# Optimization experiments

Hardware: AMD Instinct MI355X
Metric: run time of the kernel (lower is better)

The kernel has to match this reference:

```python
import jax, jax.numpy as jnp
import numpy as np

N, K, D, H, DK, DV, E = 20000, 20, 128, 4, 32, 32, 128
HID = 4 * D


def _ln(x, g, b, eps=1e-5):
    m = x.mean(-1, keepdims=True)
    v = ((x - m) ** 2).mean(-1, keepdims=True)
    return (x - m) / jnp.sqrt(v + eps) * g + b


def setup_inputs() -> dict:
    key = jax.random.key(0)
    ks = jax.random.split(key, 24)
    inp = {
        "node_h_src": jax.random.normal(ks[0], (N, K, D), jnp.float32),
        "t": jax.random.uniform(ks[1], (N, K), jnp.float32),
        "t_now": jnp.ones((1,), jnp.float32),
        "edge_feat": jax.random.normal(ks[2], (N, K, E), jnp.float32),
        # time-encoding params (as in __init__)
        "basis_freq": jnp.asarray(1.0 / 10 ** np.linspace(0, 9, D), jnp.float32),
        "phase": jnp.zeros((D,), jnp.float32),
        # edge_fc
        "edge_fc_w": jax.random.normal(ks[3], (E, D), jnp.float32) * 0.05,
        "edge_fc_b": jnp.zeros((D,), jnp.float32),
        # QKV projections (stored as [in, out])
        "w_qs": jax.random.normal(ks[4], (D, H * DK), jnp.float32) * np.sqrt(2.0 / (D + DK)),
        "w_ks": jax.random.normal(ks[5], (D, H * DK), jnp.float32) * np.sqrt(2.0 / (D + DK)),
        "w_vs": jax.random.normal(ks[6], (D, H * DV), jnp.float32) * np.sqrt(2.0 / (D + DV)),
        "w_qs_src": jax.random.normal(ks[7], (D, H * DK), jnp.float32) * np.sqrt(2.0 / (D + DK)),
        # attn output fc
        "attn_fc_w": jax.random.normal(ks[8], (H * DV, D), jnp.float32) * 0.05,
        "attn_fc_b": jnp.zeros((D,), jnp.float32),
        "attn_ln_g": jnp.ones((D,), jnp.float32),
        "attn_ln_b": jnp.zeros((D,), jnp.float32),
        # positionwise FFN (Conv1d kernel 1 == linear)
        "ffn_w1": jax.random.normal(ks[9], (D, HID), jnp.float32) * 0.05,
        "ffn_b1": jnp.zeros((HID,), jnp.float32),
        "ffn_w2": jax.random.normal(ks[10], (HID, D), jnp.float32) * 0.05,
        "ffn_b2": jnp.zeros((D,), jnp.float32),
        "ffn_ln_g": jnp.ones((D,), jnp.float32),
        "ffn_ln_b": jnp.zeros((D,), jnp.float32),
        # fuse + output norm
        "fea2node_w": jax.random.normal(ks[11], (2 * D, D), jnp.float32) * 0.05,
        "fea2node_b": jnp.zeros((D,), jnp.float32),
        "out_ln_g": jnp.ones((D,), jnp.float32),
        "out_ln_b": jnp.zeros((D,), jnp.float32),
    }
    return inp


def reference(node_h_src, t, t_now, edge_feat, basis_freq, phase,
              edge_fc_w, edge_fc_b, w_qs, w_ks, w_vs, w_qs_src,
              attn_fc_w, attn_fc_b, attn_ln_g, attn_ln_b,
              ffn_w1, ffn_b1, ffn_w2, ffn_b2, ffn_ln_g, ffn_ln_b,
              fea2node_w, fea2node_b, out_ln_g, out_ln_b):
    gelu = lambda x: jax.nn.gelu(x, approximate=False)
    # message: temporal encoding + edge feature fusion
    t_enc = jnp.cos((t_now - t)[..., None] * basis_freq + phase)          # [N,K,D]
    z = node_h_src + gelu(edge_feat @ edge_fc_w + edge_fc_b) + t_enc      # [N,K,D]
    q = z @ w_qs                                                          # [N,K,H*DK]
    k = z @ w_ks
    v = z @ w_vs
    # reduce: self message replaces last slot. NOTE: original code uses
    # self_q for q, k AND v (w_ks_src/w_vs_src unused) -- reproduced faithfully.
    self_q = (z[:, -1, :] @ w_qs_src)[:, None, :]                         # [N,1,H*DK]
    q = jnp.concatenate([q[:, :-1, :], self_q], axis=1)
    k = jnp.concatenate([k[:, :-1, :], self_q], axis=1)
    v = jnp.concatenate([v[:, :-1, :], self_q], axis=1)
    qh = q.reshape(N, K, H, DK)
    kh = k.reshape(N, K, H, DK)
    vh = v.reshape(N, K, H, DV)
    attn = jnp.einsum("nqhd,nkhd->nhqk", qh, kh) / jnp.sqrt(jnp.float32(DK))
    attn = jax.nn.softmax(attn, axis=-1)
    out = jnp.einsum("nhqk,nkhd->nqhd", attn, vh).reshape(N, K, H * DV)
    out = out @ attn_fc_w + attn_fc_b
    x = _ln(out + z, attn_ln_g, attn_ln_b)                                # [N,K,D]
    # positionwise FFN with residual + LN
    ffn = jax.nn.relu(x @ ffn_w1 + ffn_b1) @ ffn_w2 + ffn_b2
    x = _ln(ffn + x, ffn_ln_g, ffn_ln_b)
    # fuse self slot with mean of neighbor slots
    neighborhood = x[:, :-1, :].mean(axis=1)                              # [N,D]
    fused = jnp.concatenate([x[:, -1, :], neighborhood], axis=-1)         # [N,2D]
    node_h = _ln(gelu(fused @ fea2node_w + fea2node_b) + node_h_src[:, -1, :],
                 out_ln_g, out_ln_b)
    return node_h
```

## Files before the change

### kernel.cpp

```cpp
#include <hip/hip_runtime.h>
#include <hip/hip_bf16.h>

#define N_NODES 20000
#define KK 20
#define DD 128
#define HH 4
#define DKK 32
#define EE 128
#define HIDD 512
#define RTOT (N_NODES * KK)

using bf16 = __hip_bfloat16;

typedef short s16x8 __attribute__((ext_vector_type(8)));
typedef float f32x4 __attribute__((ext_vector_type(4)));

__device__ __forceinline__ float geluf(float x) {
    return 0.5f * x * (1.0f + erff(x * 0.70710678118654752f));
}

__device__ __forceinline__ float wave_sum(float v) {
#pragma unroll
    for (int o = 32; o > 0; o >>= 1) v += __shfl_down(v, o);
    return __shfl(v, 0);
}

__global__ __launch_bounds__(256)
void k0_conv(const float* __restrict__ w1, const float* __restrict__ w2,
             bf16* __restrict__ w1t, bf16* __restrict__ w2t)
{
    const int id = blockIdx.x * 256 + threadIdx.x;
    if (id < HIDD * DD) {
        const int n = id / DD, k = id % DD;
        w1t[id] = __float2bfloat16(w1[k * HIDD + n]);
    } else {
        const int j = id - HIDD * DD;
        const int n = j / HIDD, k = j % HIDD;
        w2t[j] = __float2bfloat16(w2[k * DD + n]);
    }
}

__global__ __launch_bounds__(256)
void k0b_conv(const float* __restrict__ wq, const float* __restrict__ wk,
              const float* __restrict__ wv, const float* __restrict__ wqs,
              const float* __restrict__ afw, const float* __restrict__ ew,
              bf16* __restrict__ aw)
{
    const int id = blockIdx.x * 256 + threadIdx.x;
    const int m = id >> 14;
    const int r = id & 16383;
    const int n = r >> 7, k = r & 127;
    const float* src = (m == 0) ? wq : (m == 1) ? wk : (m == 2) ? wv
                     : (m == 3) ? wqs : (m == 4) ? afw : ew;
    aw[id] = __float2bfloat16(src[k * DD + n]);
}

__global__ __launch_bounds__(256)
void k1_msg(const float* __restrict__ nhs, const float* __restrict__ t,
            const float* __restrict__ t_now, const float* __restrict__ ef,
            const float* __restrict__ freq, const float* __restrict__ phase,
            const bf16* __restrict__ ewt, const float* __restrict__ eb,
            bf16* __restrict__ z)
{
    __shared__ bf16  efs[32][136];
    __shared__ float gs[32][132];
    __shared__ float ts[32];

    const int tid  = threadIdx.x;
    const int wv   = tid >> 6;
    const int lane = tid & 63;
    const int col  = lane & 15;
    const int quad = lane >> 4;
    const size_t base = (size_t)blockIdx.x * 32 * DD;

    {
        const float4* src = (const float4*)(ef + base);
#pragma unroll
        for (int it = 0; it < 4; it++) {
            const int i = tid + it * 256;
            const int r = i >> 5, c = (i & 31) * 4;
            const float4 v = src[i];
            bf16 tmp[4] = { __float2bfloat16(v.x), __float2bfloat16(v.y),
                            __float2bfloat16(v.z), __float2bfloat16(v.w) };
            *(uint2*)&efs[r][c] = *(const uint2*)tmp;
        }
    }
    if (tid < 32) ts[tid] = t[blockIdx.x * 32 + tid];
    __syncthreads();

    {
        f32x4 acc[2][2];
#pragma unroll
        for (int mt = 0; mt < 2; mt++)
#pragma unroll
            for (int nt = 0; nt < 2; nt++) acc[mt][nt] = (f32x4){0.f, 0.f, 0.f, 0.f};

#pragma unroll
        for (int kk = 0; kk < 4; kk++) {
            const int k0 = kk * 32 + quad * 8;
            const s16x8 a0 = *(const s16x8*)&efs[col][k0];
            const s16x8 a1 = *(const s16x8*)&efs[16 + col][k0];
#pragma unroll
            for (int nt = 0; nt < 2; nt++) {
                const int n = wv * 32 + nt * 16 + col;
                const s16x8 b = *(const s16x8*)&ewt[n * DD + k0];
                acc[0][nt] = __builtin_amdgcn_mfma_f32_16x16x32_bf16(a0, b, acc[0][nt], 0, 0, 0);
                acc[1][nt] = __builtin_amdgcn_mfma_f32_16x16x32_bf16(a1, b, acc[1][nt], 0, 0, 0);
            }
        }

#pragma unroll
        for (int mt = 0; mt < 2; mt++)
#pragma unroll
            for (int nt = 0; nt < 2; nt++) {
                const int n = wv * 32 + nt * 16 + col;
                const float bias = eb[n];
#pragma unroll
                for (int r = 0; r < 4; r++) {
                    const int row = mt * 16 + quad * 4 + r;
                    gs[row][n] = geluf(acc[mt][nt][r] + bias);
                }
            }
    }
    __syncthreads();

    {
        const float tn = t_now[0];
        const float4* nsrc = (const float4*)(nhs + base);
#pragma unroll
        for (int it = 0; it < 4; it++) {
            const int i = tid + it * 256;
            const int r = i >> 5, c = (i & 31) * 4;
            const float4 h  = nsrc[i];
            const float4 fq = *(const float4*)&freq[c];
            const float4 ph = *(const float4*)&phase[c];
            const float dt  = tn - ts[r];
            const float o0 = h.x + gs[r][c + 0] + __cosf(dt * fq.x + ph.x);
            const float o1 = h.y + gs[r][c + 1] + __cosf(dt * fq.y + ph.y);
            const float o2 = h.z + gs[r][c + 2] + __cosf(dt * fq.z + ph.z);
            const float o3 = h.w + gs[r][c + 3] + __cosf(dt * fq.w + ph.w);
            bf16 o[4] = { __float2bfloat16(o0), __float2bfloat16(o1),
                          __float2bfloat16(o2), __float2bfloat16(o3) };
            *(uint2*)&z[base + r * DD + c] = *(const uint2*)o;
        }
    }
}

__global__ __launch_bounds__(256)
void k2_attn(bf16* __restrict__ zx, const bf16* __restrict__ aw,
             const float* __restrict__ afb,
             const float* __restrict__ lng, const float* __restrict__ lnb)
{
    __shared__ __align__(16) char smem[46784];
    bf16  (*zs)[136]     = (bf16  (*)[136])(smem);
    float (*qf)[132]     = (float (*)[132])(smem + 8704);
    float (*kf)[132]     = (float (*)[132])(smem + 19264);
    float (*vf)[132]     = (float (*)[132])(smem + 29824);
    float (*sc)[KK][KK]  = (float (*)[KK][KK])(smem + 40384);
    bf16  (*obf)[136]    = (bf16  (*)[136])(smem + 8704);
    float (*us)[132]     = (float (*)[132])(smem + 19264);

    const int t    = threadIdx.x;
    const int wv4  = t >> 6;
    const int lane = t & 63;
    const int col  = lane & 15;
    const int quad = lane >> 4;
    const int node = blockIdx.x;
    bf16* zrow = zx + node * KK * DD;

    const uint4 z4 = make_uint4(0u, 0u, 0u, 0u);

    {
        const uint4* src = (const uint4*)zrow;
        for (int i = t; i < 320; i += 256) {
            const int r = i >> 4, c = (i & 15) * 8;
            *(uint4*)&zs[r][c] = src[i];
        }
        for (int i = t; i < 204; i += 256) {
            const int r = 20 + i / 17, c = (i % 17) * 8;
            *(uint4*)&zs[r][c] = z4;
        }
    }
    __syncthreads();

    {
        const bf16* Wm = aw + wv4 * (DD * DD);
        f32x4 acc[2][8];
#pragma unroll
        for (int mt = 0; mt < 2; mt++)
#pragma unroll
            for (int nt = 0; nt < 8; nt++) acc[mt][nt] = (f32x4){0.f, 0.f, 0.f, 0.f};

#pragma unroll
        for (int kk = 0; kk < 4; kk++) {
            const int k0 = kk * 32 + quad * 8;
            const s16x8 a0 = *(const s16x8*)&zs[col][k0];
            const s16x8 a1 = *(const s16x8*)&zs[16 + col][k0];
#pragma unroll
            for (int nt = 0; nt < 8; nt++) {
                const s16x8 b = *(const s16x8*)&Wm[(nt * 16 + col) * DD + k0];
                acc[0][nt] = __builtin_amdgcn_mfma_f32_16x16x32_bf16(a0, b, acc[0][nt], 0, 0, 0);
                acc[1][nt] = __builtin_amdgcn_mfma_f32_16x16x32_bf16(a1, b, acc[1][nt], 0, 0, 0);
            }
        }

        if (wv4 < 3) {
            float (*dst)[132] = (wv4 == 0) ? qf : (wv4 == 1) ? kf : vf;
#pragma unroll
            for (int mt = 0; mt < 2; mt++)
#pragma unroll
                for (int nt = 0; nt < 8; nt++)
#pragma unroll
                    for (int r = 0; r < 4; r++) {
                        const int row = mt * 16 + quad * 4 + r;
                        if (row >= 19) continue;
                        dst[row][nt * 16 + col] = acc[mt][nt][r];
                    }
        } else if (quad == 0) {
#pragma unroll
            for (int nt = 0; nt < 8; nt++) {
                const int n = nt * 16 + col;
                const float s = acc[1][nt][3];
                qf[19][n] = s; kf[19][n] = s; vf[19][n] = s;
            }
        }
    }
    __syncthreads();

    const float scale = 0.17677669529663687f;
    for (int idx = t; idx < HH * KK * KK; idx += 256) {
        const int h = idx / (KK * KK);
        const int rem = idx % (KK * KK);
        const int i = rem / KK, j = rem % KK;
        float s = 0.f;
#pragma unroll
        for (int d = 0; d < DKK; d++)
            s += qf[i][h * DKK + d] * kf[j][h * DKK + d];
        sc[h][i][j] = s * scale;
    }
    __syncthreads();

    if (t < HH * KK) {
        const int h = t / KK, i = t % KK;
        float m = -1e30f;
#pragma unroll
        for (int j = 0; j < KK; j++) m = fmaxf(m, sc[h][i][j]);
        float s = 0.f;
#pragma unroll
        for (int j = 0; j < KK; j++) { const float e = __expf(sc[h][i][j] - m); sc[h][i][j] = e; s += e; }
        const float inv = 1.0f / s;
#pragma unroll
        for (int j = 0; j < KK; j++) sc[h][i][j] *= inv;
    }
    __syncthreads();

    for (int idx = t; idx < KK * DD; idx += 256) {
        const int i = idx / DD, c = idx % DD, h = c / DKK;
        float o = 0.f;
#pragma unroll
        for (int j = 0; j < KK; j++) o += sc[h][i][j] * vf[j][c];
        obf[i][c] = __float2bfloat16(o);
    }
    for (int i = t; i < 204; i += 256) {
        const int r = 20 + i / 17, c = (i % 17) * 8;
        *(uint4*)&obf[r][c] = z4;
    }
    __syncthreads();

    {
        const bf16* AF = aw + 4 * (DD * DD);
        f32x4 facc[2][2];
#pragma unroll
        for (int mt = 0; mt < 2; mt++)
#pragma unroll
            for (int nt = 0; nt < 2; nt++) facc[mt][nt] = (f32x4){0.f, 0.f, 0.f, 0.f};

#pragma unroll
        for (int kk = 0; kk < 4; kk++) {
            const int k0 = kk * 32 + quad * 8;
            const s16x8 a0 = *(const s16x8*)&obf[col][k0];
            const s16x8 a1 = *(const s16x8*)&obf[16 + col][k0];
#pragma unroll
            for (int nt = 0; nt < 2; nt++) {
                const int n = (wv4 * 2 + nt) * 16 + col;
                const s16x8 b = *(const s16x8*)&AF[n * DD + k0];
                facc[0][nt] = __builtin_amdgcn_mfma_f32_16x16x32_bf16(a0, b, facc[0][nt], 0, 0, 0);
                facc[1][nt] = __builtin_amdgcn_mfma_f32_16x16x32_bf16(a1, b, facc[1][nt], 0, 0, 0);
            }
        }

#pragma unroll
        for (int mt = 0; mt < 2; mt++)
#pragma unroll
            for (int nt = 0; nt < 2; nt++) {
                const int n = (wv4 * 2 + nt) * 16 + col;
                const float bias = afb[n];
#pragma unroll
                for (int r = 0; r < 4; r++) {
                    const int i = mt * 16 + quad * 4 + r;
                    if (i >= 20) continue;
                    us[i][n] = facc[mt][nt][r] + bias + __bfloat162float(zs[i][n]);
                }
            }
    }
    __syncthreads();

    for (int i = wv4; i < KK; i += 4) {
        const float a0 = us[i][lane], a1 = us[i][lane + 64];
        const float s  = wave_sum(a0 + a1);
        const float sq = wave_sum(a0 * a0 + a1 * a1);
        const float mean = s * (1.0f / DD);
        const float var  = sq * (1.0f / DD) - mean * mean;
        const float inv  = rsqrtf(var + 1e-5f);
        zrow[i * DD + lane]      = __float2bfloat16((a0 - mean) * inv * lng[lane] + lnb[lane]);
        zrow[i * DD + lane + 64] = __float2bfloat16((a1 - mean) * inv * lng[lane + 64] + lnb[lane + 64]);
    }
}

#define XPAD (DD + 8)
#define HPAD (HIDD + 8)

__global__ __launch_bounds__(256)
void k3_ffn(bf16* __restrict__ zx,
            const bf16* __restrict__ w1t, const float* __restrict__ b1,
            const bf16* __restrict__ w2t, const float* __restrict__ b2,
            const float* __restrict__ lng, const float* __restrict__ lnb)
{
    __shared__ bf16 xs[32][XPAD];
    __shared__ bf16 h1[32][HPAD];

    const int t    = threadIdx.x;
    const int wv   = t >> 6;
    const int lane = t & 63;
    const int col  = lane & 15;
    const int quad = lane >> 4;
    const int base = blockIdx.x * 32 * DD;

    {
        const uint4* src = (const uint4*)(zx + base);
#pragma unroll
        for (int it = 0; it < 2; it++) {
            const int i = t + it * 256;
            const int r = i >> 4, c = (i & 15) * 8;
            *(uint4*)&xs[r][c] = src[i];
        }
    }
    __syncthreads();

    {
        f32x4 acc[2][8];
#pragma unroll
        for (int mt = 0; mt < 2; mt++)
#pragma unroll
            for (int nt = 0; nt < 8; nt++) acc[mt][nt] = (f32x4){0.f, 0.f, 0.f, 0.f};

#pragma unroll
        for (int kk = 0; kk < 4; kk++) {
            const int k0 = kk * 32 + quad * 8;
            const s16x8 a0 = *(const s16x8*)&xs[col][k0];
            const s16x8 a1 = *(const s16x8*)&xs[16 + col][k0];
#pragma unroll
            for (int nt = 0; nt < 8; nt++) {
                const int n = wv * 128 + nt * 16 + col;
                const s16x8 b = *(const s16x8*)&w1t[n * DD + k0];
                acc[0][nt] = __builtin_amdgcn_mfma_f32_16x16x32_bf16(a0, b, acc[0][nt], 0, 0, 0);
                acc[1][nt] = __builtin_amdgcn_mfma_f32_16x16x32_bf16(a1, b, acc[1][nt], 0, 0, 0);
            }
        }
#pragma unroll
        for (int nt = 0; nt < 8; nt++) {
            const int n = wv * 128 + nt * 16 + col;
            const float bias = b1[n];
#pragma unroll
            for (int r = 0; r < 4; r++) {
                const int row = quad * 4 + r;
                h1[row][n]      = __float2bfloat16(fmaxf(acc[0][nt][r] + bias, 0.f));
                h1[16 + row][n] = __float2bfloat16(fmaxf(acc[1][nt][r] + bias, 0.f));
            }
        }
    }
    __syncthreads();

    {
        f32x4 acc[2][2];
#pragma unroll
        for (int mt = 0; mt < 2; mt++)
#pragma unroll
            for (int nt = 0; nt < 2; nt++) acc[mt][nt] = (f32x4){0.f, 0.f, 0.f, 0.f};

#pragma unroll 4
        for (int kk = 0; kk < 16; kk++) {
            const int k0 = kk * 32 + quad * 8;
            const s16x8 a0 = *(const s16x8*)&h1[col][k0];
            const s16x8 a1 = *(const s16x8*)&h1[16 + col][k0];
#pragma unroll
            for (int nt = 0; nt < 2; nt++) {
                const int n = wv * 32 + nt * 16 + col;
                const s16x8 b = *(const s16x8*)&w2t[n * HIDD + k0];
                acc[0][nt] = __builtin_amdgcn_mfma_f32_16x16x32_bf16(a0, b, acc[0][nt], 0, 0, 0);
                acc[1][nt] = __builtin_amdgcn_mfma_f32_16x16x32_bf16(a1, b, acc[1][nt], 0, 0, 0);
            }
        }
        __syncthreads();

        float* u = (float*)&h1[0][0];
#pragma unroll
        for (int mt = 0; mt < 2; mt++)
#pragma unroll
            for (int nt = 0; nt < 2; nt++) {
                const int n = wv * 32 + nt * 16 + col;
                const float bias = b2[n];
#pragma unroll
                for (int r = 0; r < 4; r++) {
                    const int row = mt * 16 + quad * 4 + r;
                    u[row * DD + n] = acc[mt][nt][r] + bias + __bfloat162float(xs[row][n]);
                }
            }
    }
    __syncthreads();

    {
        const float* u = (const float*)&h1[0][0];
        for (int r = wv; r < 32; r += 4) {
            const float a0 = u[r * DD + lane], a1 = u[r * DD + lane + 64];
            const float s  = wave_sum(a0 + a1);
            const float sq = wave_sum(a0 * a0 + a1 * a1);
            const float mean = s * (1.0f / DD);
            const float var  = sq * (1.0f / DD) - mean * mean;
            const float inv  = rsqrtf(var + 1e-5f);
            zx[base + r * DD + lane]      = __float2bfloat16((a0 - mean) * inv * lng[lane] + lnb[lane]);
            zx[base + r * DD + lane + 64] = __float2bfloat16((a1 - mean) * inv * lng[lane + 64] + lnb[lane + 64]);
        }
    }
}

__global__ __launch_bounds__(128)
void k4_fuse(const bf16* __restrict__ zx, const float* __restrict__ nhs,
             const float* __restrict__ fw, const float* __restrict__ fb,
             const float* __restrict__ lng, const float* __restrict__ lnb,
             float* __restrict__ out)
{
    __shared__ float f[2 * DD];
    __shared__ float red[4];
    const int d = threadIdx.x;
    const int node = blockIdx.x;
    const bf16* xr = zx + node * KK * DD;

    float nb = 0.f;
#pragma unroll
    for (int i = 0; i < KK - 1; i++) nb += __bfloat162float(xr[i * DD + d]);
    f[d] = __bfloat162float(xr[(KK - 1) * DD + d]);
    f[DD + d] = nb * (1.0f / (KK - 1));
    __syncthreads();

    float a = fb[d];
#pragma unroll 4
    for (int c = 0; c < 2 * DD; c++) a += f[c] * fw[c * DD + d];
    const float y = geluf(a) + nhs[(node * KK + KK - 1) * DD + d];

    float s = y, sq = y * y;
#pragma unroll
    for (int o = 32; o > 0; o >>= 1) {
        s += __shfl_down(s, o);
        sq += __shfl_down(sq, o);
    }
    const int wid = d >> 6, lane = d & 63;
    if (lane == 0) { red[wid] = s; red[2 + wid] = sq; }
    __syncthreads();
    const float ts = red[0] + red[1], tsq = red[2] + red[3];
    const float mean = ts * (1.0f / DD);
    const float var = tsq * (1.0f / DD) - mean * mean;
    const float inv = rsqrtf(var + 1e-5f);
    out[node * DD + d] = (y - mean) * inv * lng[d] + lnb[d];
}

extern "C" void kernel_launch(void* const* d_in, const int* in_sizes, int n_in,
                              void* d_out, int out_size, void* d_ws, size_t ws_size,
                              hipStream_t stream)
{
    const float* nhs   = (const float*)d_in[0];
    const float* t     = (const float*)d_in[1];
    const float* tnow  = (const float*)d_in[2];
    const float* ef    = (const float*)d_in[3];
    const float* freq  = (const float*)d_in[4];
    const float* phase = (const float*)d_in[5];
    const float* ew    = (const float*)d_in[6];
    const float* eb    = (const float*)d_in[7];
    const float* wq    = (const float*)d_in[8];
    const float* wk    = (const float*)d_in[9];
    const float* wv    = (const float*)d_in[10];
    const float* wqs   = (const float*)d_in[11];
    const float* afw   = (const float*)d_in[12];
    const float* afb   = (const float*)d_in[13];
    const float* alng  = (const float*)d_in[14];
    const float* alnb  = (const float*)d_in[15];
    const float* w1    = (const float*)d_in[16];
    const float* b1    = (const float*)d_in[17];
    const float* w2    = (const float*)d_in[18];
    const float* b2    = (const float*)d_in[19];
    const float* flng  = (const float*)d_in[20];
    const float* flnb  = (const float*)d_in[21];
    const float* fw    = (const float*)d_in[22];
    const float* fb    = (const float*)d_in[23];
    const float* olng  = (const float*)d_in[24];
    const float* olnb  = (const float*)d_in[25];
    float* out = (float*)d_out;

    bf16* zx  = (bf16*)d_ws;
    bf16* w1t = (bf16*)((char*)d_ws + (size_t)RTOT * DD * 2);
    bf16* w2t = w1t + HIDD * DD;
    bf16* aw  = w2t + DD * HIDD;
    bf16* ewt = aw + 5 * DD * DD;

    k0_conv<<<dim3(2 * HIDD * DD / 256), dim3(256), 0, stream>>>(w1, w2, w1t, w2t);
    k0b_conv<<<dim3(6 * DD * DD / 256), dim3(256), 0, stream>>>(wq, wk, wv, wqs, afw, ew, aw);
    k1_msg<<<dim3(RTOT / 32), dim3(256), 0, stream>>>(nhs, t, tnow, ef, freq, phase, ewt, eb, zx);
    k2_attn<<<dim3(N_NODES), dim3(256), 0, stream>>>(zx, aw, afb, alng, alnb);
    k3_ffn<<<dim3(RTOT / 32), dim3(256), 0, stream>>>(zx, w1t, b1, w2t, b2, flng, flnb);
    k4_fuse<<<dim3(N_NODES), dim3(128), 0, stream>>>(zx, nhs, fw, fb, olng, olnb, out);
}
```

Before: 1.405 ms.

## Compute attention scores and PV with MFMA in bf16, shrink shared memory

Replaces the scalar fp32 QK^T, softmax and PV loops in the attention kernel with per-head bf16 MFMA tiles, one wave per head. The softmax now runs in registers using cross-lane shuffles. Q, K and a transposed V are stored as bf16, which shrinks shared memory so a launch-bounds hint can target four blocks per CU. This adds bf16 rounding of Q, K, V and P, and padded rows 20-31 rely on whatever data is already in those shared-memory regions, which could affect correctness.

```diff
diff --git a/kernel.cpp b/kernel.cpp
--- a/kernel.cpp
+++ b/kernel.cpp
@@ -146,19 +146,19 @@
     }
 }
 
-__global__ __launch_bounds__(256)
+__global__ __launch_bounds__(256, 4)
 void k2_attn(bf16* __restrict__ zx, const bf16* __restrict__ aw,
              const float* __restrict__ afb,
              const float* __restrict__ lng, const float* __restrict__ lnb)
 {
-    __shared__ __align__(16) char smem[46784];
-    bf16  (*zs)[136]     = (bf16  (*)[136])(smem);
-    float (*qf)[132]     = (float (*)[132])(smem + 8704);
-    float (*kf)[132]     = (float (*)[132])(smem + 19264);
-    float (*vf)[132]     = (float (*)[132])(smem + 29824);
-    float (*sc)[KK][KK]  = (float (*)[KK][KK])(smem + 40384);
-    bf16  (*obf)[136]    = (bf16  (*)[136])(smem + 8704);
-    float (*us)[132]     = (float (*)[132])(smem + 19264);
+    __shared__ __align__(16) char smem[36352];
+    bf16  (*zs)[136]    = (bf16  (*)[136])(smem);
+    bf16  (*qb)[136]    = (bf16  (*)[136])(smem + 8704);
+    bf16  (*kb)[136]    = (bf16  (*)[136])(smem + 17408);
+    bf16  (*vT)[40]     = (bf16  (*)[40]) (smem + 26112);
+    bf16  (*Pm)[32][40] = (bf16  (*)[32][40])(smem + 8704);
+    bf16  (*obf)[136]   = (bf16  (*)[136])(smem + 8704);
+    float (*us)[132]    = (float (*)[132])(smem + 8704);
 
     const int t    = threadIdx.x;
     const int wv4  = t >> 6;
@@ -204,8 +204,8 @@
             }
         }
 
-        if (wv4 < 3) {
-            float (*dst)[132] = (wv4 == 0) ? qf : (wv4 == 1) ? kf : vf;
+        if (wv4 < 2) {
+            bf16 (*dst)[136] = (wv4 == 0) ? qb : kb;
 #pragma unroll
             for (int mt = 0; mt < 2; mt++)
 #pragma unroll
@@ -214,56 +214,102 @@
                     for (int r = 0; r < 4; r++) {
                         const int row = mt * 16 + quad * 4 + r;
                         if (row >= 19) continue;
-                        dst[row][nt * 16 + col] = acc[mt][nt][r];
+                        dst[row][nt * 16 + col] = __float2bfloat16(acc[mt][nt][r]);
+                    }
+        } else if (wv4 == 2) {
+#pragma unroll
+            for (int mt = 0; mt < 2; mt++)
+#pragma unroll
+                for (int nt = 0; nt < 8; nt++)
+#pragma unroll
+                    for (int r = 0; r < 4; r++) {
+                        const int row = mt * 16 + quad * 4 + r;
+                        if (row == 19) continue;
+                        vT[nt * 16 + col][row] = __float2bfloat16(acc[mt][nt][r]);
                     }
         } else if (quad == 0) {
 #pragma unroll
             for (int nt = 0; nt < 8; nt++) {
                 const int n = nt * 16 + col;
-                const float s = acc[1][nt][3];
-                qf[19][n] = s; kf[19][n] = s; vf[19][n] = s;
-            }
-        }
-    }
-    __syncthreads();
-
-    const float scale = 0.17677669529663687f;
-    for (int idx = t; idx < HH * KK * KK; idx += 256) {
-        const int h = idx / (KK * KK);
-        const int rem = idx % (KK * KK);
-        const int i = rem / KK, j = rem % KK;
-        float s = 0.f;
-#pragma unroll
-        for (int d = 0; d < DKK; d++)
-            s += qf[i][h * DKK + d] * kf[j][h * DKK + d];
-        sc[h][i][j] = s * scale;
-    }
-    __syncthreads();
-
-    if (t < HH * KK) {
-        const int h = t / KK, i = t % KK;
-        float m = -1e30f;
-#pragma unroll
-        for (int j = 0; j < KK; j++) m = fmaxf(m, sc[h][i][j]);
-        float s = 0.f;
-#pragma unroll
-        for (int j = 0; j < KK; j++) { const float e = __expf(sc[h][i][j] - m); sc[h][i][j] = e; s += e; }
-        const float inv = 1.0f / s;
-#pragma unroll
-        for (int j = 0; j < KK; j++) sc[h][i][j] *= inv;
-    }
-    __syncthreads();
-
-    for (int idx = t; idx < KK * DD; idx += 256) {
-        const int i = idx / DD, c = idx % DD, h = c / DKK;
-        float o = 0.f;
-#pragma unroll
-        for (int j = 0; j < KK; j++) o += sc[h][i][j] * vf[j][c];
-        obf[i][c] = __float2bfloat16(o);
-    }
-    for (int i = t; i < 204; i += 256) {
-        const int r = 20 + i / 17, c = (i % 17) * 8;
-        *(uint4*)&obf[r][c] = z4;
+                const bf16 s = __float2bfloat16(acc[1][nt][3]);
+                qb[19][n] = s; kb[19][n] = s; vT[n][19] = s;
+            }
+        }
+    }
+    __syncthreads();
+
+    float p0[2][4], p1[2][4];
+    {
+        const int hb = wv4 * DKK;
+        const int k0 = quad * 8;
+        const s16x8 qa0 = *(const s16x8*)&qb[col][hb + k0];
+        const s16x8 qa1 = *(const s16x8*)&qb[16 + col][hb + k0];
+        const s16x8 kf0 = *(const s16x8*)&kb[col][hb + k0];
+        const s16x8 kf1 = *(const s16x8*)&kb[16 + col][hb + k0];
+        const f32x4 zero = (f32x4){0.f, 0.f, 0.f, 0.f};
+        f32x4 sacc[2][2];
+        sacc[0][0] = __builtin_amdgcn_mfma_f32_16x16x32_bf16(qa0, kf0, zero, 0, 0, 0);
+        sacc[0][1] = __builtin_amdgcn_mfma_f32_16x16x32_bf16(qa0, kf1, zero, 0, 0, 0);
+        sacc[1][0] = __builtin_amdgcn_mfma_f32_16x16x32_bf16(qa1, kf0, zero, 0, 0, 0);
+        sacc[1][1] = __builtin_amdgcn_mfma_f32_16x16x32_bf16(qa1, kf1, zero, 0, 0, 0);
+
+        const float scale = 0.17677669529663687f;
+#pragma unroll
+        for (int mt = 0; mt < 2; mt++)
+#pragma unroll
+            for (int r = 0; r < 4; r++) {
+                const float s0 = sacc[mt][0][r] * scale;
+                const float s1 = sacc[mt][1][r] * scale;
+                float mx = fmaxf(s0, (col < 4) ? s1 : -1e30f);
+#pragma unroll
+                for (int o = 1; o < 16; o <<= 1) mx = fmaxf(mx, __shfl_xor(mx, o));
+                const float e0 = __expf(s0 - mx);
+                const float e1 = (col < 4) ? __expf(s1 - mx) : 0.f;
+                float sm = e0 + e1;
+#pragma unroll
+                for (int o = 1; o < 16; o <<= 1) sm += __shfl_xor(sm, o);
+                const float inv = 1.0f / sm;
+                p0[mt][r] = e0 * inv;
+                p1[mt][r] = e1 * inv;
+            }
+    }
+    __syncthreads();
+
+#pragma unroll
+    for (int mt = 0; mt < 2; mt++)
+#pragma unroll
+        for (int r = 0; r < 4; r++) {
+            const int i = mt * 16 + quad * 4 + r;
+            Pm[wv4][i][col]      = __float2bfloat16(p0[mt][r]);
+            Pm[wv4][i][16 + col] = __float2bfloat16(p1[mt][r]);
+        }
+
+    f32x4 oacc[2][2];
+    {
+        const int hb = wv4 * DKK;
+        const int k0 = quad * 8;
+        const s16x8 pa0 = *(const s16x8*)&Pm[wv4][col][k0];
+        const s16x8 pa1 = *(const s16x8*)&Pm[wv4][16 + col][k0];
+        const s16x8 vb0 = *(const s16x8*)&vT[hb + col][k0];
+        const s16x8 vb1 = *(const s16x8*)&vT[hb + 16 + col][k0];
+        const f32x4 zero = (f32x4){0.f, 0.f, 0.f, 0.f};
+        oacc[0][0] = __builtin_amdgcn_mfma_f32_16x16x32_bf16(pa0, vb0, zero, 0, 0, 0);
+        oacc[0][1] = __builtin_amdgcn_mfma_f32_16x16x32_bf16(pa0, vb1, zero, 0, 0, 0);
+        oacc[1][0] = __builtin_amdgcn_mfma_f32_16x16x32_bf16(pa1, vb0, zero, 0, 0, 0);
+        oacc[1][1] = __builtin_amdgcn_mfma_f32_16x16x32_bf16(pa1, vb1, zero, 0, 0, 0);
+    }
+    __syncthreads();
+
+    {
+        const int hb = wv4 * DKK;
+#pragma unroll
+        for (int mt = 0; mt < 2; mt++)
+#pragma unroll
+            for (int nt = 0; nt < 2; nt++)
+#pragma unroll
+                for (int r = 0; r < 4; r++)
+                    obf[mt * 16 + quad * 4 + r][hb + nt * 16 + col] =
+                        __float2bfloat16(oacc[mt][nt][r]);
     }
     __syncthreads();
 
@@ -288,6 +334,7 @@
                 facc[1][nt] = __builtin_amdgcn_mfma_f32_16x16x32_bf16(a1, b, facc[1][nt], 0, 0, 0);
             }
         }
+        __syncthreads();
 
 #pragma unroll
         for (int mt = 0; mt < 2; mt++)
```

New measurement: 1.367 ms. -2.7%, faster.
